# Performance work log

Measured on AMD Instinct MI355X. Metric: run time of the kernel, lower is better.

## Reference

```python
import jax, jax.numpy as jnp
import numpy as np

ALPHA = 0.7
BETA = 0.3
GAMMA = 1.0
EPS = 1e-07


def setup_inputs() -> dict:
    key = jax.random.key(0)
    k1, k2 = jax.random.split(key)
    B, C, H, W = 8, 19, 512, 512
    inputs = jax.random.normal(k1, (B, C, H, W), dtype=jnp.float32)
    targets = jax.random.randint(k2, (B, H, W), 0, C, dtype=jnp.int64)
    return {"inputs": inputs, "targets": targets}


def reference(inputs, targets):
    # inputs: [B, C, H, W] logits; targets: [B, H, W] int labels
    B, C = inputs.shape[0], inputs.shape[1]
    probs = jax.nn.softmax(inputs, axis=1)  # [B, C, H, W]
    # one-hot target per class: [B, C, H, W]
    tgt = (targets[:, None, :, :] == jnp.arange(C)[None, :, None, None]).astype(probs.dtype)
    # per (b, c) reductions over spatial dims
    TP = jnp.sum(probs * tgt, axis=(2, 3))          # [B, C]
    FP = jnp.sum((1.0 - tgt) * probs, axis=(2, 3))  # [B, C]
    FN = jnp.sum(tgt * (1.0 - probs), axis=(2, 3))  # [B, C]
    tversky = (TP + EPS) / (TP + ALPHA * FN + BETA * FP + EPS)
    focal_tversky = (1.0 - tversky) ** GAMMA
    return jnp.sum(focal_tversky) / B
```

## Files before the change

### kernel.cpp

```cpp
#include <hip/hip_runtime.h>

#define NCLS 19
#define HWPIX (512 * 512)
#define NB 8
#define ALPHA_C 0.7f
#define BETA_C 0.3f
#define EPS_C 1e-7f

__global__ __launch_bounds__(256, 3) void ftl_reduce(
    const float* __restrict__ x,
    const int* __restrict__ tgt,
    float* __restrict__ part,
    int PB) {
  const int b = blockIdx.x / PB;
  const int blk = blockIdx.x % PB;
  const int tid = threadIdx.x;

  const int quadsPerBlock = (HWPIX / 4) / PB;
  const int qbase = blk * quadsPerBlock;

  const float* xb = x + (size_t)b * NCLS * HWPIX;
  const int* tb = tgt + (size_t)b * HWPIX;

  float S[NCLS], TP[NCLS];
  int Nw[NCLS];
#pragma unroll
  for (int c = 0; c < NCLS; ++c) { S[c] = 0.f; TP[c] = 0.f; Nw[c] = 0; }

  for (int q = tid; q < quadsPerBlock; q += 256) {
    const int pix = (qbase + q) * 4;
    float4 xv[NCLS];
#pragma unroll
    for (int c = 0; c < NCLS; ++c)
      xv[c] = *reinterpret_cast<const float4*>(xb + (size_t)c * HWPIX + pix);
    const int4 t = *reinterpret_cast<const int4*>(tb + pix);

    float4 se = make_float4(0.f, 0.f, 0.f, 0.f);
#pragma unroll
    for (int c = 0; c < NCLS; ++c) {
      xv[c].x = __expf(xv[c].x); se.x += xv[c].x;
      xv[c].y = __expf(xv[c].y); se.y += xv[c].y;
      xv[c].z = __expf(xv[c].z); se.z += xv[c].z;
      xv[c].w = __expf(xv[c].w); se.w += xv[c].w;
    }
    const float4 inv = make_float4(__builtin_amdgcn_rcpf(se.x),
                                   __builtin_amdgcn_rcpf(se.y),
                                   __builtin_amdgcn_rcpf(se.z),
                                   __builtin_amdgcn_rcpf(se.w));
#pragma unroll
    for (int c = 0; c < NCLS; ++c) {
      const float px_ = xv[c].x * inv.x;
      const float py_ = xv[c].y * inv.y;
      const float pz_ = xv[c].z * inv.z;
      const float pw_ = xv[c].w * inv.w;
      const bool ex = (t.x == c), ey = (t.y == c), ez = (t.z == c), ew = (t.w == c);
      S[c] += (px_ + py_) + (pz_ + pw_);
      TP[c] += ((ex ? px_ : 0.f) + (ey ? py_ : 0.f)) +
               ((ez ? pz_ : 0.f) + (ew ? pw_ : 0.f));
      Nw[c] += (int)__popcll(__ballot(ex)) + (int)__popcll(__ballot(ey)) +
               (int)__popcll(__ballot(ez)) + (int)__popcll(__ballot(ew));
    }
  }

#pragma unroll
  for (int c = 0; c < NCLS; ++c) {
    for (int off = 32; off; off >>= 1) {
      S[c] += __shfl_down(S[c], off);
      TP[c] += __shfl_down(TP[c], off);
    }
  }

  __shared__ float sS[NCLS], sTP[NCLS];
  __shared__ int sN[NCLS];
  if (tid < NCLS) { sS[tid] = 0.f; sTP[tid] = 0.f; sN[tid] = 0; }
  __syncthreads();
  if ((tid & 63) == 0) {
#pragma unroll
    for (int c = 0; c < NCLS; ++c) {
      atomicAdd(&sS[c], S[c]);
      atomicAdd(&sTP[c], TP[c]);
      atomicAdd(&sN[c], Nw[c]);
    }
  }
  __syncthreads();
  if (tid < NCLS) {
    float* p = part + (size_t)blockIdx.x * (3 * NCLS);
    p[tid] = sS[tid];
    p[NCLS + tid] = sTP[tid];
    p[2 * NCLS + tid] = (float)sN[tid];
  }
}

__global__ __launch_bounds__(640) void ftl_final(
    const float* __restrict__ part, float* __restrict__ out, int PB) {
  const int tid = threadIdx.x;
  const int pair = tid >> 2;
  const int s = tid & 3;
  float v = 0.f;
  if (pair < NB * NCLS) {
    const int b = pair / NCLS;
    const int c = pair % NCLS;
    float S = 0.f, TP = 0.f, Nc = 0.f;
    for (int p = s; p < PB; p += 4) {
      const float* q = part + (size_t)(b * PB + p) * (3 * NCLS);
      S += q[c];
      TP += q[NCLS + c];
      Nc += q[2 * NCLS + c];
    }
    S += __shfl_xor(S, 1);  S += __shfl_xor(S, 2);
    TP += __shfl_xor(TP, 1); TP += __shfl_xor(TP, 2);
    Nc += __shfl_xor(Nc, 1); Nc += __shfl_xor(Nc, 2);
    if (s == 0) {
      const float FPv = S - TP;
      const float FNv = Nc - TP;
      const float tv = (TP + EPS_C) / (TP + ALPHA_C * FNv + BETA_C * FPv + EPS_C);
      v = 1.0f - tv;
    }
  }
  for (int off = 32; off; off >>= 1) v += __shfl_down(v, off);
  __shared__ float wsum[10];
  if ((tid & 63) == 0) wsum[tid >> 6] = v;
  __syncthreads();
  if (tid == 0) {
    float r = 0.f;
#pragma unroll
    for (int w = 0; w < 10; ++w) r += wsum[w];
    out[0] = r / (float)NB;
  }
}

extern "C" void kernel_launch(void* const* d_in, const int* in_sizes, int n_in,
                              void* d_out, int out_size, void* d_ws, size_t ws_size,
                              hipStream_t stream) {
  const float* x = (const float*)d_in[0];
  const int* tgt = (const int*)d_in[1];
  float* out = (float*)d_out;
  float* part = (float*)d_ws;

  int PB = 128;
  while (PB > 1 && (size_t)(NB * PB * 3 * NCLS * sizeof(float)) > ws_size) PB >>= 1;

  ftl_reduce<<<NB * PB, 256, 0, stream>>>(x, tgt, part, PB);
  ftl_final<<<1, 640, 0, stream>>>(part, out, PB);
}
```

Before: 56.79 us.

## Gather target logit and use LDS atomics for TP/count instead of per-class masks

After: 61.51 us. +8.3%, slower.

```diff
diff --git a/kernel.cpp b/kernel.cpp
--- a/kernel.cpp
+++ b/kernel.cpp
@@ -6,6 +6,9 @@
 #define ALPHA_C 0.7f
 #define BETA_C 0.3f
 #define EPS_C 1e-7f
+#define L2E 1.44269504088896f
+
+typedef float v2f __attribute__((ext_vector_type(2)));
 
 __global__ __launch_bounds__(256, 3) void ftl_reduce(
     const float* __restrict__ x,
@@ -16,71 +19,61 @@
   const int blk = blockIdx.x % PB;
   const int tid = threadIdx.x;
 
+  __shared__ float sS[NCLS], sTP[NCLS];
+  __shared__ int sN[NCLS];
+  if (tid < NCLS) { sS[tid] = 0.f; sTP[tid] = 0.f; sN[tid] = 0; }
+  __syncthreads();
+
   const int quadsPerBlock = (HWPIX / 4) / PB;
   const int qbase = blk * quadsPerBlock;
-
   const float* xb = x + (size_t)b * NCLS * HWPIX;
   const int* tb = tgt + (size_t)b * HWPIX;
 
-  float S[NCLS], TP[NCLS];
-  int Nw[NCLS];
+  v2f S2[NCLS];
 #pragma unroll
-  for (int c = 0; c < NCLS; ++c) { S[c] = 0.f; TP[c] = 0.f; Nw[c] = 0; }
+  for (int c = 0; c < NCLS; ++c) S2[c] = (v2f){0.f, 0.f};
 
   for (int q = tid; q < quadsPerBlock; q += 256) {
     const int pix = (qbase + q) * 4;
-    float4 xv[NCLS];
+    const int4 t = *reinterpret_cast<const int4*>(tb + pix);
+    const float xt0 = xb[(size_t)t.x * HWPIX + pix + 0];
+    const float xt1 = xb[(size_t)t.y * HWPIX + pix + 1];
+    const float xt2 = xb[(size_t)t.z * HWPIX + pix + 2];
+    const float xt3 = xb[(size_t)t.w * HWPIX + pix + 3];
+
+    v2f ea[NCLS], eb[NCLS];
+    v2f sea = (v2f){0.f, 0.f}, seb = (v2f){0.f, 0.f};
+#pragma unroll
+    for (int c = 0; c < NCLS; ++c) {
+      const float4 xv = *reinterpret_cast<const float4*>(xb + (size_t)c * HWPIX + pix);
+      v2f a = (v2f){xv.x, xv.y} * L2E;
+      v2f bb = (v2f){xv.z, xv.w} * L2E;
+      ea[c] = (v2f){__builtin_amdgcn_exp2f(a.x), __builtin_amdgcn_exp2f(a.y)};
+      eb[c] = (v2f){__builtin_amdgcn_exp2f(bb.x), __builtin_amdgcn_exp2f(bb.y)};
+      sea += ea[c];
+      seb += eb[c];
+    }
+    const v2f inva = (v2f){__builtin_amdgcn_rcpf(sea.x), __builtin_amdgcn_rcpf(sea.y)};
+    const v2f invb = (v2f){__builtin_amdgcn_rcpf(seb.x), __builtin_amdgcn_rcpf(seb.y)};
 #pragma unroll
     for (int c = 0; c < NCLS; ++c)
-      xv[c] = *reinterpret_cast<const float4*>(xb + (size_t)c * HWPIX + pix);
-    const int4 t = *reinterpret_cast<const int4*>(tb + pix);
+      S2[c] += ea[c] * inva + eb[c] * invb;
 
-    float4 se = make_float4(0.f, 0.f, 0.f, 0.f);
-#pragma unroll
-    for (int c = 0; c < NCLS; ++c) {
-      xv[c].x = __expf(xv[c].x); se.x += xv[c].x;
-      xv[c].y = __expf(xv[c].y); se.y += xv[c].y;
-      xv[c].z = __expf(xv[c].z); se.z += xv[c].z;
-      xv[c].w = __expf(xv[c].w); se.w += xv[c].w;
-    }
-    const float4 inv = make_float4(__builtin_amdgcn_rcpf(se.x),
-                                   __builtin_amdgcn_rcpf(se.y),
-                                   __builtin_amdgcn_rcpf(se.z),
-                                   __builtin_amdgcn_rcpf(se.w));
-#pragma unroll
-    for (int c = 0; c < NCLS; ++c) {
-      const float px_ = xv[c].x * inv.x;
-      const float py_ = xv[c].y * inv.y;
-      const float pz_ = xv[c].z * inv.z;
-      const float pw_ = xv[c].w * inv.w;
-      const bool ex = (t.x == c), ey = (t.y == c), ez = (t.z == c), ew = (t.w == c);
-      S[c] += (px_ + py_) + (pz_ + pw_);
-      TP[c] += ((ex ? px_ : 0.f) + (ey ? py_ : 0.f)) +
-               ((ez ? pz_ : 0.f) + (ew ? pw_ : 0.f));
-      Nw[c] += (int)__popcll(__ballot(ex)) + (int)__popcll(__ballot(ey)) +
-               (int)__popcll(__ballot(ez)) + (int)__popcll(__ballot(ew));
-    }
+    atomicAdd(&sTP[t.x], __builtin_amdgcn_exp2f(xt0 * L2E) * inva.x);
+    atomicAdd(&sTP[t.y], __builtin_amdgcn_exp2f(xt1 * L2E) * inva.y);
+    atomicAdd(&sTP[t.z], __builtin_amdgcn_exp2f(xt2 * L2E) * invb.x);
+    atomicAdd(&sTP[t.w], __builtin_amdgcn_exp2f(xt3 * L2E) * invb.y);
+    atomicAdd(&sN[t.x], 1);
+    atomicAdd(&sN[t.y], 1);
+    atomicAdd(&sN[t.z], 1);
+    atomicAdd(&sN[t.w], 1);
   }
 
 #pragma unroll
   for (int c = 0; c < NCLS; ++c) {
-    for (int off = 32; off; off >>= 1) {
-      S[c] += __shfl_down(S[c], off);
-      TP[c] += __shfl_down(TP[c], off);
-    }
-  }
-
-  __shared__ float sS[NCLS], sTP[NCLS];
-  __shared__ int sN[NCLS];
-  if (tid < NCLS) { sS[tid] = 0.f; sTP[tid] = 0.f; sN[tid] = 0; }
-  __syncthreads();
-  if ((tid & 63) == 0) {
-#pragma unroll
-    for (int c = 0; c < NCLS; ++c) {
-      atomicAdd(&sS[c], S[c]);
-      atomicAdd(&sTP[c], TP[c]);
-      atomicAdd(&sN[c], Nw[c]);
-    }
+    float Sc = S2[c].x + S2[c].y;
+    for (int off = 32; off; off >>= 1) Sc += __shfl_down(Sc, off);
+    if ((tid & 63) == 0) atomicAdd(&sS[c], Sc);
   }
   __syncthreads();
   if (tid < NCLS) {
```
